# Performance work log

Measured on AMD Instinct MI355X. Metric: run time of the kernel, lower is better.

The kernel has to match this reference:

```python
import jax, jax.numpy as jnp
import numpy as np

EMBED_DIM = 1024
NUM_HEADS = 16
HEAD_DIM = EMBED_DIM // NUM_HEADS


def setup_inputs() -> dict:
    key = jax.random.key(0)
    ks = jax.random.split(key, 9)
    B, S, D = 2, 2048, EMBED_DIM
    scale = 1.0 / np.sqrt(D)
    x = jax.random.normal(ks[0], (B, S, D), dtype=jnp.float32)
    # nn.Linear weights are [out, in]; store as [in, out] for x @ W
    Wq = jax.random.uniform(ks[1], (D, D), jnp.float32, -scale, scale)
    bq = jax.random.uniform(ks[2], (D,), jnp.float32, -scale, scale)
    Wk = jax.random.uniform(ks[3], (D, D), jnp.float32, -scale, scale)
    bk = jax.random.uniform(ks[4], (D,), jnp.float32, -scale, scale)
    Wv = jax.random.uniform(ks[5], (D, D), jnp.float32, -scale, scale)
    bv = jax.random.uniform(ks[6], (D,), jnp.float32, -scale, scale)
    Wo = jax.random.uniform(ks[7], (D, D), jnp.float32, -scale, scale)
    bo = jax.random.uniform(ks[8], (D,), jnp.float32, -scale, scale)
    return {"x": x, "Wq": Wq, "bq": bq, "Wk": Wk, "bk": bk,
            "Wv": Wv, "bv": bv, "Wo": Wo, "bo": bo}


def reference(x, Wq, bq, Wk, bk, Wv, bv, Wo, bo):
    B, S, D = x.shape
    H, Dh = NUM_HEADS, HEAD_DIM
    q = (x @ Wq + bq).reshape(B, S, H, Dh).transpose(0, 2, 1, 3)  # [B,H,S,Dh]
    k = (x @ Wk + bk).reshape(B, S, H, Dh).transpose(0, 2, 1, 3)
    v = (x @ Wv + bv).reshape(B, S, H, Dh).transpose(0, 2, 1, 3)
    scores = jnp.einsum('bhqd,bhkd->bhqk', q, k) / jnp.sqrt(jnp.float32(Dh))
    attn = jax.nn.softmax(scores, axis=-1)
    out = jnp.einsum('bhqk,bhkd->bhqd', attn, v)  # [B,H,S,Dh]
    out = out.transpose(0, 2, 1, 3).reshape(B, S, D)
    return out @ Wo + bo
```

## Files before the change

### kernel.cpp

```cpp
#include <hip/hip_runtime.h>
#include <hip/hip_bf16.h>
#include <stdint.h>

using f32x4 = __attribute__((ext_vector_type(4))) float;
using s16x8 = __attribute__((ext_vector_type(8))) short;
using s16x4 = __attribute__((ext_vector_type(4))) short;

__device__ __forceinline__ unsigned short f2bf(float f) {
  union { float f; unsigned int u; } v; v.f = f;
  return (unsigned short)((v.u + 0x7FFFu + ((v.u >> 16) & 1u)) >> 16);
}

__device__ __forceinline__ float exp2_(float x) {
  float r;
  asm("v_exp_f32 %0, %1" : "=v"(r) : "v"(x));
  return r;
}

__device__ __forceinline__ s16x4 pk4(float a, float b, float c, float d) {
  union { unsigned u[2]; s16x4 v; } r;
  asm("v_cvt_pk_bf16_f32 %0, %1, %2" : "=v"(r.u[0]) : "v"(a), "v"(b));
  asm("v_cvt_pk_bf16_f32 %0, %1, %2" : "=v"(r.u[1]) : "v"(c), "v"(d));
  return r.v;
}

__device__ __forceinline__ short pbf(float f) {
  __hip_bfloat16 h = __float2bfloat16(f);
  return *(short*)&h;
}

#define GLD16(gp, lp) __builtin_amdgcn_global_load_lds( \
    (const __attribute__((address_space(1))) unsigned int*)(uintptr_t)(gp), \
    (__attribute__((address_space(3))) unsigned int*)(uintptr_t)(lp), 16, 0, 0)

__device__ __forceinline__ f32x4 mfma32(s16x8 a, s16x8 b, f32x4 c) {
  return __builtin_amdgcn_mfma_f32_16x16x32_bf16(a, b, c, 0, 0, 0);
}

#if __has_builtin(__builtin_amdgcn_mfma_f32_16x16x16bf16_1k)
__device__ __forceinline__ f32x4 mfma16(s16x4 a, s16x4 b, f32x4 c) {
  return __builtin_amdgcn_mfma_f32_16x16x16bf16_1k(a, b, c, 0, 0, 0);
}
#else
__device__ __forceinline__ f32x4 mfma16(s16x4 a, s16x4 b, f32x4 c) {
  f32x4 d;
  asm volatile("v_mfma_f32_16x16x16_bf16 %0, %1, %2, %3"
               : "=v"(d) : "v"(a), "v"(b), "v"(c));
  return d;
}
#endif

__global__ __launch_bounds__(256)
void prep(const float* __restrict__ x,
          const float* __restrict__ Wq, const float* __restrict__ Wk,
          const float* __restrict__ Wv, const float* __restrict__ Wo,
          unsigned short* __restrict__ xb, unsigned short* __restrict__ Wt) {
  __shared__ float tile[64][65];
  int blk = blockIdx.x;
  int tid = threadIdx.x;
  if (blk < 1024) {
    const float4* xi = (const float4*)x;
    ushort4* xo = (ushort4*)xb;
    #pragma unroll
    for (int j = 0; j < 4; ++j) {
      int i = blk * 1024 + j * 256 + tid;
      float4 v = xi[i];
      ushort4 o;
      o.x = f2bf(v.x); o.y = f2bf(v.y); o.z = f2bf(v.z); o.w = f2bf(v.w);
      xo[i] = o;
    }
  } else {
    int wid = blk - 1024;
    int which = wid >> 8, t = wid & 255;
    const float* W = (which == 0) ? Wq : (which == 1) ? Wk : (which == 2) ? Wv : Wo;
    unsigned short* dst = Wt + (size_t)which * 1048576;
    int k0 = (t & 15) * 64, n0 = (t >> 4) * 64;
    int tx = tid & 63, ty = tid >> 6;
    #pragma unroll
    for (int j = 0; j < 64; j += 4)
      tile[ty + j][tx] = W[(size_t)(k0 + ty + j) * 1024 + n0 + tx];
    __syncthreads();
    #pragma unroll
    for (int j = 0; j < 64; j += 4)
      dst[(size_t)(n0 + ty + j) * 1024 + k0 + tx] = f2bf(tile[tx][ty + j]);
  }
}

__global__ __launch_bounds__(256)
void qkv_gemm(const unsigned short* __restrict__ A,
              const unsigned short* __restrict__ Bt,
              const float* __restrict__ bq, const float* __restrict__ bk,
              const float* __restrict__ bv,
              unsigned short* __restrict__ qo, unsigned short* __restrict__ kf,
              unsigned short* __restrict__ vf) {
  __shared__ unsigned short ldsA[2][4096];
  __shared__ unsigned short ldsB[2][4096];
  int orig = blockIdx.x;
  int wg = (orig & 7) * 96 + (orig >> 3);
  int bm = wg / 24;
  int bn = wg - bm * 24;
  int m0 = bm << 7, n0 = bn << 7;
  int tid = threadIdx.x;
  int w = tid >> 6, ln = tid & 63;
  int g = ln >> 4, c = ln & 15;
  int wr = w >> 1, wc = w & 1;

  const unsigned short* ga = A + (size_t)(m0 + (tid >> 2)) * 1024 + (tid & 3) * 8;
  const unsigned short* gb = Bt + (size_t)(n0 + (tid >> 2)) * 1024 + (tid & 3) * 8;
  int lb = w * 512;

  f32x4 acc[4][4];
  f32x4 zero = {0.f, 0.f, 0.f, 0.f};
  #pragma unroll
  for (int m = 0; m < 4; ++m)
    #pragma unroll
    for (int n = 0; n < 4; ++n) acc[m][n] = zero;

  GLD16(ga, &ldsA[0][lb]);
  GLD16(ga + 65536, &ldsA[0][2048 + lb]);
  GLD16(gb, &ldsB[0][lb]);
  GLD16(gb + 65536, &ldsB[0][2048 + lb]);
  __syncthreads();

  int aoff = (wr * 64 + c) * 32 + g * 8;
  int boff = (wc * 64 + c) * 32 + g * 8;

  int cur = 0;
  for (int t = 0; t < 32; ++t) {
    if (t < 31) {
      const unsigned short* ga2 = ga + (t + 1) * 32;
      const unsigned short* gb2 = gb + (t + 1) * 32;
      int nb = cur ^ 1;
      GLD16(ga2, &ldsA[nb][lb]);
      GLD16(ga2 + 65536, &ldsA[nb][2048 + lb]);
      GLD16(gb2, &ldsB[nb][lb]);
      GLD16(gb2 + 65536, &ldsB[nb][2048 + lb]);
    }
    s16x8 af[4], bf[4];
    #pragma unroll
    for (int m = 0; m < 4; ++m)
      af[m] = *(const s16x8*)&ldsA[cur][aoff + m * 512];
    #pragma unroll
    for (int n = 0; n < 4; ++n)
      bf[n] = *(const s16x8*)&ldsB[cur][boff + n * 512];
    #pragma unroll
    for (int m = 0; m < 4; ++m)
      #pragma unroll
      for (int n = 0; n < 4; ++n)
        acc[m][n] = mfma32(af[m], bf[n], acc[m][n]);
    __syncthreads();
    cur ^= 1;
  }

  #pragma unroll
  for (int n = 0; n < 4; ++n) {
    int cg = n0 + wc * 64 + n * 16 + c;
    int p = cg >> 10;
    int d = cg & 1023;
    int hh = d >> 6, dh = d & 63;
    const float* bp = (p == 0) ? bq : (p == 1) ? bk : bv;
    float bias = bp[d];
    #pragma unroll
    for (int m = 0; m < 4; ++m) {
      int r = m0 + wr * 64 + m * 16 + g * 4;
      int b = r >> 11, s = r & 2047;
      size_t pv = (size_t)((b << 4) + hh);
      if (p == 2) {
        int T = s >> 4;
        int Tp = T >> 1, par = T & 1;
        int dtp = dh >> 4;
        ushort4 pk;
        pk.x = f2bf(acc[m][n][0] + bias);
        pk.y = f2bf(acc[m][n][1] + bias);
        pk.z = f2bf(acc[m][n][2] + bias);
        pk.w = f2bf(acc[m][n][3] + bias);
        *(ushort4*)&vf[pv * 131072 +
                       (size_t)(((Tp * 4 + dtp) * 64 + g * 16 + c) * 8 + par * 4)] = pk;
      } else if (p == 1) {
        int T = s >> 4;
        int h2 = dh >> 5, gp = (dh >> 3) & 3, j = dh & 7;
        unsigned short* kd = kf + pv * 131072 + T * 1024 + h2 * 512 +
                             (gp * 16 + (s & 15)) * 8 + j;
        kd[0]  = f2bf(acc[m][n][0] + bias);
        kd[8]  = f2bf(acc[m][n][1] + bias);
        kd[16] = f2bf(acc[m][n][2] + bias);
        kd[24] = f2bf(acc[m][n][3] + bias);
      } else {
        const float sc = 0.180336880111120f;
        size_t base = (pv * 2048 + s) * 64 + dh;
        qo[base]       = f2bf((acc[m][n][0] + bias) * sc);
        qo[base + 64]  = f2bf((acc[m][n][1] + bias) * sc);
        qo[base + 128] = f2bf((acc[m][n][2] + bias) * sc);
        qo[base + 192] = f2bf((acc[m][n][3] + bias) * sc);
      }
    }
  }
}

__global__ __launch_bounds__(256, 2)
void attn_fwd(const unsigned short* __restrict__ q,
              const unsigned short* __restrict__ kfb,
              const unsigned short* __restrict__ vfb,
              unsigned short* __restrict__ ao) {
  __shared__ unsigned short ldsKV[3][8192];
  int orig = blockIdx.x;
  int wg = (orig & 7) * 64 + (orig >> 3);
  int pair = wg >> 4, qt = wg & 15;
  int tid = threadIdx.x;
  int w = tid >> 6, ln = tid & 63;
  int g = ln >> 4, c = ln & 15;
  int q0 = qt * 128 + w * 32;
  const unsigned short* qp = q + (size_t)pair * 131072;
  const char* kbase = (const char*)(kfb + (size_t)pair * 131072);
  const char* vbase = (const char*)(vfb + (size_t)pair * 131072);

  const char* ssrc = ((w < 2) ? kbase : vbase) + (w & 1) * 4096;
  int dsto = (w >= 2 ? 8192 : 0) + (w & 1) * 4096;

  s16x8 qf[2][2];
  #pragma unroll
  for (int j = 0; j < 2; ++j)
    #pragma unroll
    for (int h = 0; h < 2; ++h)
      qf[j][h] = *(const s16x8*)&qp[(q0 + j * 16 + c) * 64 + h * 32 + g * 8];

  f32x4 acc[2][4];
  f32x4 zero = {0.f, 0.f, 0.f, 0.f};
  #pragma unroll
  for (int j = 0; j < 2; ++j)
    #pragma unroll
    for (int dt = 0; dt < 4; ++dt) acc[j][dt] = zero;
  float l0 = 0.f, l1 = 0.f;

  #pragma unroll
  for (int j = 0; j < 4; ++j)
    GLD16(ssrc + j * 1024 + ln * 16, (char*)&ldsKV[0][0] + dsto + j * 1024);

  const unsigned short* L0 = ldsKV[0];
  const unsigned short* L1 = ldsKV[1];
  const unsigned short* L2 = ldsKV[2];
  s16x4 paA[2][4], paB[2][4];

#define ATTN_ITER(T, LC, LP, LN, PAC, PAP)                                     \
  {                                                                            \
    if ((T) < 31) {                                                            \
      const char* s2 = ssrc + ((T) + 1) * 8192;                                \
      char* d2 = (char*)(LN) + dsto;                                           \
      _Pragma("unroll")                                                        \
      for (int j = 0; j < 4; ++j)                                              \
        GLD16(s2 + j * 1024 + ln * 16, d2 + j * 1024);                         \
      asm volatile("s_waitcnt vmcnt(4)" ::: "memory");                         \
    } else {                                                                   \
      asm volatile("s_waitcnt vmcnt(0)" ::: "memory");                         \
    }                                                                          \
    __builtin_amdgcn_s_barrier();                                              \
                                    \
    s16x8 kc[4][2];                                                            \
    _Pragma("unroll")                                                          \
    for (int kt = 0; kt < 4; ++kt) {                                           \
      kc[kt][0] = *(const s16x8*)&(LC)[kt * 1024 + ln * 8];                    \
      kc[kt][1] = *(const s16x8*)&(LC)[kt * 1024 + 512 + ln * 8];              \
    }                                                                          \
    f32x4 st[4][2];                                                            \
    __builtin_amdgcn_s_setprio(1);                                             \
    _Pragma("unroll")                                                          \
    for (int kt = 0; kt < 4; ++kt)                                             \
      _Pragma("unroll")                                                        \
      for (int j = 0; j < 2; ++j) {                                            \
        f32x4 t2 = zero;                                                       \
        t2 = mfma32(kc[kt][0], qf[j][0], t2);                                  \
        t2 = mfma32(kc[kt][1], qf[j][1], t2);                                  \
        st[kt][j] = t2;                                                        \
      }                                                                        \
    __builtin_amdgcn_s_setprio(0);                                             \
                 \
    if ((T) > 0) {                                                             \
      __builtin_amdgcn_s_setprio(1);                                           \
      _Pragma("unroll")                                                        \
      for (int dt = 0; dt < 4; ++dt)                                           \
        _Pragma("unroll")                                                      \
        for (int tp = 0; tp < 2; ++tp) {                                       \
          s16x8 vv = *(const s16x8*)&(LP)[4096 + tp * 2048 + dt * 512 + ln * 8]; \
          s16x4 vlo = __builtin_shufflevector(vv, vv, 0, 1, 2, 3);             \
          s16x4 vhi = __builtin_shufflevector(vv, vv, 4, 5, 6, 7);             \
          _Pragma("unroll")                                                    \
          for (int j = 0; j < 2; ++j) {                                        \
            acc[j][dt] = mfma16((PAP)[j][tp * 2], vlo, acc[j][dt]);            \
            acc[j][dt] = mfma16((PAP)[j][tp * 2 + 1], vhi, acc[j][dt]);        \
          }                                                                    \
        }                                                                      \
      __builtin_amdgcn_s_setprio(0);                                           \
    }                                                                          \
                              \
    _Pragma("unroll")                                                          \
    for (int kt = 0; kt < 4; ++kt) {                                           \
      float p00 = exp2_(st[kt][0][0]), p01 = exp2_(st[kt][0][1]);              \
      float p02 = exp2_(st[kt][0][2]), p03 = exp2_(st[kt][0][3]);              \
      float p10 = exp2_(st[kt][1][0]), p11 = exp2_(st[kt][1][1]);              \
      float p12 = exp2_(st[kt][1][2]), p13 = exp2_(st[kt][1][3]);              \
      l0 += (p00 + p01) + (p02 + p03);                                         \
      l1 += (p10 + p11) + (p12 + p13);                                         \
      (PAC)[0][kt] = pk4(p00, p01, p02, p03);                                  \
      (PAC)[1][kt] = pk4(p10, p11, p12, p13);                                  \
    }                                                                          \
    __builtin_amdgcn_s_barrier();                                              \
  }

  for (int t = 0; t < 32; t += 2) {
    ATTN_ITER(t,     L0, L2, L1, paA, paB);
    ATTN_ITER(t + 1, L1, L0, L2, paB, paA);
    const unsigned short* tmp = L2;
    L2 = L1; L1 = L0; L0 = tmp;
  }
#undef ATTN_ITER

  __builtin_amdgcn_s_setprio(1);
  #pragma unroll
  for (int dt = 0; dt < 4; ++dt)
    #pragma unroll
    for (int tp = 0; tp < 2; ++tp) {
      s16x8 vv = *(const s16x8*)&L2[4096 + tp * 2048 + dt * 512 + ln * 8];
      s16x4 vlo = __builtin_shufflevector(vv, vv, 0, 1, 2, 3);
      s16x4 vhi = __builtin_shufflevector(vv, vv, 4, 5, 6, 7);
      #pragma unroll
      for (int j = 0; j < 2; ++j) {
        acc[j][dt] = mfma16(paB[j][tp * 2], vlo, acc[j][dt]);
        acc[j][dt] = mfma16(paB[j][tp * 2 + 1], vhi, acc[j][dt]);
      }
    }
  __builtin_amdgcn_s_setprio(0);

  l0 += __shfl_xor(l0, 16); l0 += __shfl_xor(l0, 32);
  l1 += __shfl_xor(l1, 16); l1 += __shfl_xor(l1, 32);
  float li0 = 1.f / l0, li1 = 1.f / l1;
  int b = pair >> 4, hh = pair & 15;
  #pragma unroll
  for (int e = 0; e < 4; ++e) {
    float i0 = __shfl(li0, g * 4 + e);
    float i1 = __shfl(li1, g * 4 + e);
    size_t r0 = ((size_t)(b * 2048 + q0 + g * 4 + e) * 16 + hh) * 64;
    size_t r1 = ((size_t)(b * 2048 + q0 + 16 + g * 4 + e) * 16 + hh) * 64;
    #pragma unroll
    for (int dt = 0; dt < 4; ++dt) {
      ao[r0 + dt * 16 + c] = (unsigned short)pbf(acc[0][dt][e] * i0);
      ao[r1 + dt * 16 + c] = (unsigned short)pbf(acc[1][dt][e] * i1);
    }
  }
}

__global__ __launch_bounds__(256)
void out_gemm(const unsigned short* __restrict__ A,
              const unsigned short* __restrict__ Bt,
              const float* __restrict__ bo, float* __restrict__ out) {
  __shared__ unsigned short lds[2][6144];
  int orig = blockIdx.x;
  int wg = (orig & 7) * 64 + (orig >> 3);
  int bm = wg >> 3, bn = wg & 7;
  int m0 = bm << 6, n0 = bn << 7;
  int tid = threadIdx.x;
  int w = tid >> 6, ln = tid & 63;
  int g = ln >> 4, c = ln & 15;
  int wr = w >> 1, wc = w & 1;

  const unsigned short* su[3];
  int du[3];
  #pragma unroll
  for (int i = 0; i < 3; ++i) {
    int u = 3 * w + i;
    if (u < 4) {
      su[i] = A + (size_t)(m0 + u * 16 + (ln >> 2)) * 1024 + (ln & 3) * 8;
      du[i] = u * 512;
    } else {
      int v2 = u - 4;
      su[i] = Bt + (size_t)(n0 + v2 * 16 + (ln >> 2)) * 1024 + (ln & 3) * 8;
      du[i] = 2048 + v2 * 512;
    }
  }

  f32x4 acc[2][4];
  f32x4 zero = {0.f, 0.f, 0.f, 0.f};
  #pragma unroll
  for (int m = 0; m < 2; ++m)
    #pragma unroll
    for (int n = 0; n < 4; ++n) acc[m][n] = zero;

  #pragma unroll
  for (int i = 0; i < 3; ++i) GLD16(su[i], &lds[0][du[i]]);
  __syncthreads();

  int aoff = (wr * 32 + c) * 32 + g * 8;
  int boff = 2048 + (wc * 64 + c) * 32 + g * 8;

  int cur = 0;
  for (int t = 0; t < 32; ++t) {
    if (t < 31) {
      int nb = cur ^ 1;
      #pragma unroll
      for (int i = 0; i < 3; ++i) GLD16(su[i] + (t + 1) * 32, &lds[nb][du[i]]);
    }
    s16x8 af[2], bf[4];
    #pragma unroll
    for (int m = 0; m < 2; ++m)
      af[m] = *(const s16x8*)&lds[cur][aoff + m * 512];
    #pragma unroll
    for (int n = 0; n < 4; ++n)
      bf[n] = *(const s16x8*)&lds[cur][boff + n * 512];
    #pragma unroll
    for (int m = 0; m < 2; ++m)
      #pragma unroll
      for (int n = 0; n < 4; ++n)
        acc[m][n] = mfma32(af[m], bf[n], acc[m][n]);
    __syncthreads();
    cur ^= 1;
  }

  #pragma unroll
  for (int n = 0; n < 4; ++n) {
    int cg = n0 + wc * 64 + n * 16 + c;
    float bias = bo[cg];
    #pragma unroll
    for (int m = 0; m < 2; ++m) {
      int r = m0 + wr * 32 + m * 16 + g * 4;
      out[(size_t)r * 1024 + cg] = acc[m][n][0] + bias;
      out[(size_t)(r + 1) * 1024 + cg] = acc[m][n][1] + bias;
      out[(size_t)(r + 2) * 1024 + cg] = acc[m][n][2] + bias;
      out[(size_t)(r + 3) * 1024 + cg] = acc[m][n][3] + bias;
    }
  }
}

extern "C" void kernel_launch(void* const* d_in, const int* in_sizes, int n_in,
                              void* d_out, int out_size, void* d_ws, size_t ws_size,
                              hipStream_t stream) {
  (void)in_sizes; (void)n_in; (void)out_size; (void)ws_size;
  const float* x  = (const float*)d_in[0];
  const float* Wq = (const float*)d_in[1];
  const float* bq = (const float*)d_in[2];
  const float* Wk = (const float*)d_in[3];
  const float* bk = (const float*)d_in[4];
  const float* Wv = (const float*)d_in[5];
  const float* bv = (const float*)d_in[6];
  const float* Wo = (const float*)d_in[7];
  const float* bo = (const float*)d_in[8];
  float* out = (float*)d_out;
  char* ws = (char*)d_ws;
  unsigned short* xb  = (unsigned short*)(ws);
  unsigned short* Wt  = (unsigned short*)(ws + 8388608);
  unsigned short* Wot = (unsigned short*)(ws + 14680064);
  unsigned short* qb  = (unsigned short*)(ws + 16777216);
  unsigned short* kfb = (unsigned short*)(ws + 25165824);
  unsigned short* vfb = (unsigned short*)(ws + 33554432);
  unsigned short* ao  = (unsigned short*)(ws + 41943040);

  prep<<<2048, 256, 0, stream>>>(x, Wq, Wk, Wv, Wo, xb, Wt);
  qkv_gemm<<<768, 256, 0, stream>>>(xb, Wt, bq, bk, bv, qb, kfb, vfb);
  attn_fwd<<<512, 256, 0, stream>>>(qb, kfb, vfb, ao);
  out_gemm<<<512, 256, 0, stream>>>(ao, Wot, bo, out);
}
```

Baseline: 111.4 us.

## Retile QKV GEMM to 256x256 blocks with 8 waves and swizzled LDS

The QKV projection GEMM moves from 128x128 tiles with 4 waves and a K-step of 32 to 256x256 tiles with 8 waves, a K-step of 64 and 192 workgroups. LDS loads use an XOR swizzle to avoid bank conflicts, and the per-wave MFMA work is ordered to reuse A/B fragments. The goal is to raise arithmetic intensity and cut global/LDS traffic per FLOP. In exchange, 192 blocks on a 256-CU part leave some CUs idle, and the larger register footprint (128 accumulator floats per lane) may reduce occupancy.

```diff
diff --git a/kernel.cpp b/kernel.cpp
--- a/kernel.cpp
+++ b/kernel.cpp
@@ -86,94 +86,148 @@
   }
 }
 
-__global__ __launch_bounds__(256)
+__global__ __launch_bounds__(512, 2)
 void qkv_gemm(const unsigned short* __restrict__ A,
               const unsigned short* __restrict__ Bt,
               const float* __restrict__ bq, const float* __restrict__ bk,
               const float* __restrict__ bv,
               unsigned short* __restrict__ qo, unsigned short* __restrict__ kf,
               unsigned short* __restrict__ vf) {
-  __shared__ unsigned short ldsA[2][4096];
-  __shared__ unsigned short ldsB[2][4096];
+  __shared__ unsigned short lds2[2][32768];
   int orig = blockIdx.x;
-  int wg = (orig & 7) * 96 + (orig >> 3);
-  int bm = wg / 24;
-  int bn = wg - bm * 24;
-  int m0 = bm << 7, n0 = bn << 7;
+  int wg = (orig & 7) * 24 + (orig >> 3);
+  int bm = wg / 12, bn = wg % 12;
+  int m0 = bm << 8, n0 = bn << 8;
   int tid = threadIdx.x;
   int w = tid >> 6, ln = tid & 63;
   int g = ln >> 4, c = ln & 15;
-  int wr = w >> 1, wc = w & 1;
-
-  const unsigned short* ga = A + (size_t)(m0 + (tid >> 2)) * 1024 + (tid & 3) * 8;
-  const unsigned short* gb = Bt + (size_t)(n0 + (tid >> 2)) * 1024 + (tid & 3) * 8;
-  int lb = w * 512;
-
-  f32x4 acc[4][4];
+  int wm = w >> 2, wn = w & 3;
+
+  int rrs = tid >> 3;
+  int lcol = (((tid & 7) ^ ((tid >> 3) & 7)) << 4);
+  const char* pA = (const char*)A + (size_t)(m0 + rrs) * 2048 + lcol;
+  const char* pB = (const char*)Bt + (size_t)(n0 + rrs) * 2048 + lcol;
+  int woff = w * 1024;
+
+#define QKV_STAGE(buf, kt)                                                     \
+  {                                                                            \
+    char* db = (char*)&lds2[buf][0];                                           \
+    _Pragma("unroll")                                                          \
+    for (int h = 0; h < 2; ++h)                                                \
+      _Pragma("unroll")                                                        \
+      for (int i = 0; i < 2; ++i) {                                            \
+        GLD16(pA + (size_t)(h * 128 + i * 64) * 2048 + (kt) * 128,             \
+              db + h * 16384 + i * 8192 + woff);                               \
+        GLD16(pB + (size_t)(h * 128 + i * 64) * 2048 + (kt) * 128,             \
+              db + 32768 + h * 16384 + i * 8192 + woff);                       \
+      }                                                                        \
+  }
+
+  int cs = (c & 7) << 4;
+#define DSF(Lp, row, kk) \
+  (*(const s16x8*)&(Lp)[(row) * 64 + ((((kk) * 64 + g * 16) ^ cs) >> 1)])
+
+  f32x4 acc[8][4];
   f32x4 zero = {0.f, 0.f, 0.f, 0.f};
   #pragma unroll
-  for (int m = 0; m < 4; ++m)
-    #pragma unroll
-    for (int n = 0; n < 4; ++n) acc[m][n] = zero;
-
-  GLD16(ga, &ldsA[0][lb]);
-  GLD16(ga + 65536, &ldsA[0][2048 + lb]);
-  GLD16(gb, &ldsB[0][lb]);
-  GLD16(gb + 65536, &ldsB[0][2048 + lb]);
-  __syncthreads();
-
-  int aoff = (wr * 64 + c) * 32 + g * 8;
-  int boff = (wc * 64 + c) * 32 + g * 8;
-
-  int cur = 0;
-  for (int t = 0; t < 32; ++t) {
-    if (t < 31) {
-      const unsigned short* ga2 = ga + (t + 1) * 32;
-      const unsigned short* gb2 = gb + (t + 1) * 32;
-      int nb = cur ^ 1;
-      GLD16(ga2, &ldsA[nb][lb]);
-      GLD16(ga2 + 65536, &ldsA[nb][2048 + lb]);
-      GLD16(gb2, &ldsB[nb][lb]);
-      GLD16(gb2 + 65536, &ldsB[nb][2048 + lb]);
-    }
-    s16x8 af[4], bf[4];
-    #pragma unroll
-    for (int m = 0; m < 4; ++m)
-      af[m] = *(const s16x8*)&ldsA[cur][aoff + m * 512];
-    #pragma unroll
-    for (int n = 0; n < 4; ++n)
-      bf[n] = *(const s16x8*)&ldsB[cur][boff + n * 512];
-    #pragma unroll
-    for (int m = 0; m < 4; ++m)
-      #pragma unroll
-      for (int n = 0; n < 4; ++n)
-        acc[m][n] = mfma32(af[m], bf[n], acc[m][n]);
-    __syncthreads();
-    cur ^= 1;
-  }
-
-  #pragma unroll
-  for (int n = 0; n < 4; ++n) {
-    int cg = n0 + wc * 64 + n * 16 + c;
+  for (int mi = 0; mi < 8; ++mi)
+    #pragma unroll
+    for (int ni = 0; ni < 4; ++ni) acc[mi][ni] = zero;
+
+  QKV_STAGE(0, 0);
+  asm volatile("s_waitcnt vmcnt(0)" ::: "memory");
+  __builtin_amdgcn_s_barrier();
+
+  for (int kt = 0; kt < 16; ++kt) {
+    int bsel = kt & 1;
+    const unsigned short* LA = &lds2[bsel][wm * 8192];
+    const unsigned short* LB = &lds2[bsel][16384 + (wn >> 1) * 8192];
+    int rB = (wn & 1) * 64;
+    if (kt < 15) QKV_STAGE(bsel ^ 1, kt + 1);
+
+    s16x8 a[4][2], b0[2][2], b1[2][2];
+    #pragma unroll
+    for (int mi = 0; mi < 4; ++mi) {
+      a[mi][0] = DSF(LA, mi * 16 + c, 0);
+      a[mi][1] = DSF(LA, mi * 16 + c, 1);
+    }
+    #pragma unroll
+    for (int ni = 0; ni < 2; ++ni) {
+      b0[ni][0] = DSF(LB, rB + ni * 16 + c, 0);
+      b0[ni][1] = DSF(LB, rB + ni * 16 + c, 1);
+    }
+    #pragma unroll
+    for (int mi = 0; mi < 4; ++mi)
+      #pragma unroll
+      for (int ni = 0; ni < 2; ++ni) {
+        acc[mi][ni] = mfma32(a[mi][0], b0[ni][0], acc[mi][ni]);
+        acc[mi][ni] = mfma32(a[mi][1], b0[ni][1], acc[mi][ni]);
+      }
+    #pragma unroll
+    for (int mi = 0; mi < 4; ++mi) {
+      a[mi][0] = DSF(LA, (mi + 4) * 16 + c, 0);
+      a[mi][1] = DSF(LA, (mi + 4) * 16 + c, 1);
+    }
+    #pragma unroll
+    for (int mi = 0; mi < 4; ++mi)
+      #pragma unroll
+      for (int ni = 0; ni < 2; ++ni) {
+        acc[mi + 4][ni] = mfma32(a[mi][0], b0[ni][0], acc[mi + 4][ni]);
+        acc[mi + 4][ni] = mfma32(a[mi][1], b0[ni][1], acc[mi + 4][ni]);
+      }
+    #pragma unroll
+    for (int ni = 0; ni < 2; ++ni) {
+      b1[ni][0] = DSF(LB, rB + (ni + 2) * 16 + c, 0);
+      b1[ni][1] = DSF(LB, rB + (ni + 2) * 16 + c, 1);
+    }
+    #pragma unroll
+    for (int mi = 0; mi < 4; ++mi)
+      #pragma unroll
+      for (int ni = 0; ni < 2; ++ni) {
+        acc[mi + 4][ni + 2] = mfma32(a[mi][0], b1[ni][0], acc[mi + 4][ni + 2]);
+        acc[mi + 4][ni + 2] = mfma32(a[mi][1], b1[ni][1], acc[mi + 4][ni + 2]);
+      }
+    #pragma unroll
+    for (int mi = 0; mi < 4; ++mi) {
+      a[mi][0] = DSF(LA, mi * 16 + c, 0);
+      a[mi][1] = DSF(LA, mi * 16 + c, 1);
+    }
+    #pragma unroll
+    for (int mi = 0; mi < 4; ++mi)
+      #pragma unroll
+      for (int ni = 0; ni < 2; ++ni) {
+        acc[mi][ni + 2] = mfma32(a[mi][0], b1[ni][0], acc[mi][ni + 2]);
+        acc[mi][ni + 2] = mfma32(a[mi][1], b1[ni][1], acc[mi][ni + 2]);
+      }
+
+    asm volatile("s_waitcnt vmcnt(0)" ::: "memory");
+    __builtin_amdgcn_s_barrier();
+  }
+#undef QKV_STAGE
+#undef DSF
+
+  #pragma unroll
+  for (int ni = 0; ni < 4; ++ni) {
+    int cg = n0 + wn * 64 + ni * 16 + c;
     int p = cg >> 10;
     int d = cg & 1023;
     int hh = d >> 6, dh = d & 63;
     const float* bp = (p == 0) ? bq : (p == 1) ? bk : bv;
     float bias = bp[d];
     #pragma unroll
-    for (int m = 0; m < 4; ++m) {
-      int r = m0 + wr * 64 + m * 16 + g * 4;
-      int b = r >> 11, s = r & 2047;
-      size_t pv = (size_t)((b << 4) + hh);
+    for (int mi = 0; mi < 8; ++mi) {
+      int r = m0 + wm * 128 + mi * 16 + g * 4;
+      int b2 = r >> 11, s = r & 2047;
+      size_t pv = (size_t)((b2 << 4) + hh);
       if (p == 2) {
         int T = s >> 4;
         int Tp = T >> 1, par = T & 1;
         int dtp = dh >> 4;
         ushort4 pk;
-        pk.x = f2bf(acc[m][n][0] + bias);
-        pk.y = f2bf(acc[m][n][1] + bias);
-        pk.z = f2bf(acc[m][n][2] + bias);
-        pk.w = f2bf(acc[m][n][3] + bias);
+        pk.x = f2bf(acc[mi][ni][0] + bias);
+        pk.y = f2bf(acc[mi][ni][1] + bias);
+        pk.z = f2bf(acc[mi][ni][2] + bias);
+        pk.w = f2bf(acc[mi][ni][3] + bias);
         *(ushort4*)&vf[pv * 131072 +
                        (size_t)(((Tp * 4 + dtp) * 64 + g * 16 + c) * 8 + par * 4)] = pk;
       } else if (p == 1) {
@@ -181,17 +235,17 @@
         int h2 = dh >> 5, gp = (dh >> 3) & 3, j = dh & 7;
         unsigned short* kd = kf + pv * 131072 + T * 1024 + h2 * 512 +
                              (gp * 16 + (s & 15)) * 8 + j;
-        kd[0]  = f2bf(acc[m][n][0] + bias);
-        kd[8]  = f2bf(acc[m][n][1] + bias);
-        kd[16] = f2bf(acc[m][n][2] + bias);
-        kd[24] = f2bf(acc[m][n][3] + bias);
+        kd[0]  = f2bf(acc[mi][ni][0] + bias);
+        kd[8]  = f2bf(acc[mi][ni][1] + bias);
+        kd[16] = f2bf(acc[mi][ni][2] + bias);
+        kd[24] = f2bf(acc[mi][ni][3] + bias);
       } else {
         const float sc = 0.180336880111120f;
         size_t base = (pv * 2048 + s) * 64 + dh;
-        qo[base]       = f2bf((acc[m][n][0] + bias) * sc);
-        qo[base + 64]  = f2bf((acc[m][n][1] + bias) * sc);
-        qo[base + 128] = f2bf((acc[m][n][2] + bias) * sc);
-        qo[base + 192] = f2bf((acc[m][n][3] + bias) * sc);
+        qo[base]       = f2bf((acc[mi][ni][0] + bias) * sc);
+        qo[base + 64]  = f2bf((acc[mi][ni][1] + bias) * sc);
+        qo[base + 128] = f2bf((acc[mi][ni][2] + bias) * sc);
+        qo[base + 192] = f2bf((acc[mi][ni][3] + bias) * sc);
       }
     }
   }
@@ -254,7 +308,6 @@
       asm volatile("s_waitcnt vmcnt(0)" ::: "memory");                         \
     }                                                                          \
     __builtin_amdgcn_s_barrier();                                              \
-                                    \
     s16x8 kc[4][2];                                                            \
     _Pragma("unroll")                                                          \
     for (int kt = 0; kt < 4; ++kt) {                                           \
@@ -273,7 +326,6 @@
         st[kt][j] = t2;                                                        \
       }                                                                        \
     __builtin_amdgcn_s_setprio(0);                                             \
-                 \
     if ((T) > 0) {                                                             \
       __builtin_amdgcn_s_setprio(1);                                           \
       _Pragma("unroll")                                                        \
@@ -291,7 +343,6 @@
         }                                                                      \
       __builtin_amdgcn_s_setprio(0);                                           \
     }                                                                          \
-                              \
     _Pragma("unroll")                                                          \
     for (int kt = 0; kt < 4; ++kt) {                                           \
       float p00 = exp2_(st[kt][0][0]), p01 = exp2_(st[kt][0][1]);              \
@@ -453,7 +504,7 @@
   unsigned short* ao  = (unsigned short*)(ws + 41943040);
 
   prep<<<2048, 256, 0, stream>>>(x, Wq, Wk, Wv, Wo, xb, Wt);
-  qkv_gemm<<<768, 256, 0, stream>>>(xb, Wt, bq, bk, bv, qb, kfb, vfb);
+  qkv_gemm<<<192, 512, 0, stream>>>(xb, Wt, bq, bk, bv, qb, kfb, vfb);
   attn_fwd<<<512, 256, 0, stream>>>(qb, kfb, vfb, ao);
   out_gemm<<<512, 256, 0, stream>>>(ao, Wot, bo, out);
 }
```

Result: faster. 105.1 us (-5.6%).
